# Kernel tuning notes

Measured on AMD Instinct MI355X. Metric: run time of the kernel, lower is better.

Reference implementation:

```python
import jax, jax.numpy as jnp
import numpy as np

N = 100000      # nodes
E = 1600000     # edges (avg degree 16)
EP = 500000     # pos/neg scored edges
DIN, DH, DOUT = 128, 128, 64


def setup_inputs() -> dict:
    key = jax.random.key(0)
    ks = jax.random.split(key, 8)
    x = jax.random.normal(ks[0], (N, DIN), jnp.float32)
    edge_index = jax.random.randint(ks[1], (2, E), 0, N)
    pos_edge_index = jax.random.randint(ks[2], (2, EP), 0, N)
    neg_edge_index = jax.random.randint(ks[3], (2, EP), 0, N)
    s = lambda k, sh: jax.random.normal(k, sh, jnp.float32) * 0.05
    return dict(
        x=x, edge_index=edge_index,
        pos_edge_index=pos_edge_index, neg_edge_index=neg_edge_index,
        W_l0=s(ks[4], (DIN, DH)), b_l0=jnp.zeros((DH,), jnp.float32), W_r0=s(ks[5], (DIN, DH)),
        W_l1=s(ks[6], (DH, DOUT)), b_l1=jnp.zeros((DOUT,), jnp.float32), W_r1=s(ks[7], (DH, DOUT)),
    )


def sage_conv(h, src, dst, W_l, b_l, W_r):
    # PyG SAGEConv (mean aggr): out_i = W_l @ mean_{j in N(i)} h_j + b_l + W_r @ h_i
    msg = h[src]                                                   # [E, d] gather
    agg = jax.ops.segment_sum(msg, dst, num_segments=h.shape[0])   # [N, d]
    deg = jax.ops.segment_sum(jnp.ones((src.shape[0],), h.dtype), dst, num_segments=h.shape[0])
    mean = agg / jnp.maximum(deg, 1.0)[:, None]
    return mean @ W_l + b_l + h @ W_r


def reference(x, edge_index, pos_edge_index, neg_edge_index,
              W_l0, b_l0, W_r0, W_l1, b_l1, W_r1):
    src, dst = edge_index[0], edge_index[1]
    h = sage_conv(x, src, dst, W_l0, b_l0, W_r0)
    h = jax.nn.relu(h)          # dropout is identity in eval mode
    h = sage_conv(h, src, dst, W_l1, b_l1, W_r1)
    pos_scores = (h[pos_edge_index[0]] * h[pos_edge_index[1]]).sum(axis=1)
    neg_scores = (h[neg_edge_index[0]] * h[neg_edge_index[1]]).sum(axis=1)
    return (pos_scores, neg_scores)
```

## Files before the change

kernel.cpp:

```cpp
#include <hip/hip_runtime.h>

#define NN 100000
#define EE 1600000
#define EPE 500000
#define NBINS 196
#define BCAP 12288
#define EPB 4096
#define NB1 391

typedef short bf8_t __attribute__((ext_vector_type(8)));
typedef float f4_t  __attribute__((ext_vector_type(4)));

__device__ __forceinline__ unsigned short f2bf(float f) {
    unsigned u = __float_as_uint(f);
    unsigned r = (u + 0x7fffu + ((u >> 16) & 1u)) >> 16;
    return (unsigned short)r;
}
__device__ __forceinline__ float bfl(unsigned u) { return __uint_as_float(u << 16); }
__device__ __forceinline__ float bfh(unsigned u) { return __uint_as_float(u & 0xffff0000u); }

__global__ __launch_bounds__(256) void binpass1_k(
    const int* __restrict__ src, const int* __restrict__ dst,
    int* __restrict__ bin_cnt, int* __restrict__ binbuf)
{
    __shared__ int cnt_l[NBINS];
    __shared__ int base_l[NBINS];
    int tid = threadIdx.x;
    int e0 = blockIdx.x * EPB;
    for (int i = tid; i < NBINS; i += 256) cnt_l[i] = 0;
    __syncthreads();

    int pk[16];
    #pragma unroll
    for (int i = 0; i < 16; ++i) {
        int e = e0 + tid + i * 256;
        pk[i] = -1;
        if (e < EE) {
            int b = dst[e] >> 9;
            int r = atomicAdd(&cnt_l[b], 1);
            pk[i] = (b << 16) | r;
        }
    }
    __syncthreads();
    for (int i = tid; i < NBINS; i += 256)
        base_l[i] = atomicAdd(&bin_cnt[i], cnt_l[i]);
    __syncthreads();

    #pragma unroll
    for (int i = 0; i < 16; ++i) {
        int e = e0 + tid + i * 256;
        if (e >= EE) continue;
        int b = pk[i] >> 16, r = pk[i] & 0xFFFF;
        int d = dst[e], s = src[e];
        binbuf[b * BCAP + base_l[b] + r] = ((d & 511) << 17) | s;
    }
}

__global__ void binscan_k(const int* __restrict__ bin_cnt, int* __restrict__ bin_base) {
    __shared__ int s[256];
    int tid = threadIdx.x;
    int v = (tid < NBINS) ? bin_cnt[tid] : 0;
    s[tid] = v;
    __syncthreads();
    #pragma unroll
    for (int off = 1; off < 256; off <<= 1) {
        int t = (tid >= off) ? s[tid - off] : 0;
        __syncthreads();
        s[tid] += t;
        __syncthreads();
    }
    if (tid < NBINS) bin_base[tid] = s[tid] - v;
}

__global__ __launch_bounds__(256) void binpass2_k(
    const int* __restrict__ binbuf, const int* __restrict__ bin_cnt,
    const int* __restrict__ bin_base, int* __restrict__ csr,
    int* __restrict__ row_ptr, float* __restrict__ invd)
{
    __shared__ int deg_l[512];
    __shared__ int off_l[512];
    __shared__ int cur_l[512];
    __shared__ int s[256];
    int tid = threadIdx.x;
    int b = blockIdx.x;
    int lo = b << 9;
    int n_here = min(512, NN - lo);
    int cnt = bin_cnt[b];
    int base = bin_base[b];
    const int* bb = binbuf + b * BCAP;

    deg_l[tid] = 0; deg_l[tid + 256] = 0;
    __syncthreads();
    for (int i = tid; i < cnt; i += 256)
        atomicAdd(&deg_l[bb[i] >> 17], 1);
    __syncthreads();

    int a0 = deg_l[2 * tid], a1 = deg_l[2 * tid + 1];
    s[tid] = a0 + a1;
    __syncthreads();
    #pragma unroll
    for (int off = 1; off < 256; off <<= 1) {
        int t = (tid >= off) ? s[tid - off] : 0;
        __syncthreads();
        s[tid] += t;
        __syncthreads();
    }
    int excl = s[tid] - (a0 + a1);
    off_l[2 * tid] = excl;
    off_l[2 * tid + 1] = excl + a0;
    cur_l[2 * tid] = excl;
    cur_l[2 * tid + 1] = excl + a0;
    __syncthreads();

    for (int j = tid; j < n_here; j += 256) {
        row_ptr[lo + j] = base + off_l[j];
        invd[lo + j] = 1.0f / fmaxf((float)deg_l[j], 1.0f);
    }
    if (tid == 0 && b == NBINS - 1) row_ptr[NN] = EE;

    for (int i = tid; i < cnt; i += 256) {
        int v = bb[i];
        int dstl = v >> 17, srcv = v & 0x1FFFF;
        int pos = atomicAdd(&cur_l[dstl], 1);
        csr[base + pos] = srcv;
    }
}

__global__ void pack_b_k(const float* __restrict__ Wl, const float* __restrict__ Wr,
                         int ncl, int ntot, unsigned short* __restrict__ Bp) {
    int t = blockIdx.x * 256 + threadIdx.x;
    if (t >= 4 * ntot * 4) return;
    int q = t & 3;
    int n = (t >> 2) % ntot;
    int kt = t / (4 * ntot);
    int ncr = ntot - ncl;
    unsigned short o[8];
    #pragma unroll
    for (int j = 0; j < 8; ++j) {
        int k = kt * 32 + q * 8 + j;
        float v = (n < ncl) ? Wl[(size_t)k * ncl + n] : Wr[(size_t)k * ncr + (n - ncl)];
        o[j] = f2bf(v);
    }
    uint4 w;
    w.x = (unsigned)o[0] | ((unsigned)o[1] << 16);
    w.y = (unsigned)o[2] | ((unsigned)o[3] << 16);
    w.z = (unsigned)o[4] | ((unsigned)o[5] << 16);
    w.w = (unsigned)o[6] | ((unsigned)o[7] << 16);
    *(uint4*)(Bp + (size_t)t * 8) = w;
}

template<int NCOLS, int TCOLS, bool AFP32>
__global__ __launch_bounds__(256) void gemm_k(
    const void* __restrict__ Av, const unsigned short* __restrict__ Bp,
    unsigned short* __restrict__ Tout, unsigned short* __restrict__ Rout)
{
    constexpr int NT = NCOLS / 16;
    int wave = threadIdx.x >> 6;
    int lane = threadIdx.x & 63;
    int ln = lane & 15, q = lane >> 4;
    int row0 = (blockIdx.x * 4 + wave) * 16;
    if (row0 >= NN) return;
    int arow = row0 + ln;

    f4_t acc[NT];
    #pragma unroll
    for (int nt = 0; nt < NT; ++nt) acc[nt] = (f4_t){0.f, 0.f, 0.f, 0.f};

    #pragma unroll
    for (int kt = 0; kt < 4; ++kt) {
        bf8_t a;
        if (AFP32) {
            const float* ap = (const float*)Av + (size_t)arow * 128 + kt * 32 + q * 8;
            f4_t a0 = *(const f4_t*)ap;
            f4_t a1 = *(const f4_t*)(ap + 4);
            #pragma unroll
            for (int j = 0; j < 4; ++j) {
                a[j]     = (short)f2bf(a0[j]);
                a[4 + j] = (short)f2bf(a1[j]);
            }
        } else {
            a = *(const bf8_t*)((const unsigned short*)Av + (size_t)arow * 128 + kt * 32 + q * 8);
        }
        const unsigned short* bb = Bp + (size_t)kt * NCOLS * 32 + (size_t)ln * 32 + q * 8;
        #pragma unroll
        for (int nt = 0; nt < NT; ++nt) {
            bf8_t b = *(const bf8_t*)(bb + nt * 512);
            acc[nt] = __builtin_amdgcn_mfma_f32_16x16x32_bf16(a, b, acc[nt], 0, 0, 0);
        }
    }

    #pragma unroll
    for (int nt = 0; nt < NT; ++nt) {
        #pragma unroll
        for (int r = 0; r < 4; ++r) {
            int row = row0 + q * 4 + r;
            int col = nt * 16 + ln;
            unsigned short v = f2bf(acc[nt][r]);
            if (col < TCOLS) Tout[(size_t)row * TCOLS + col] = v;
            else             Rout[(size_t)row * (NCOLS - TCOLS) + (col - TCOLS)] = v;
        }
    }
}

template<int LPNS, int WIDTH, bool RELU>
__global__ void gather_fuse_k(const unsigned short* __restrict__ feat,
                              const int* __restrict__ csr, const int* __restrict__ row_ptr,
                              const float* __restrict__ invd,
                              const unsigned short* __restrict__ rterm,
                              const float* __restrict__ bias,
                              unsigned short* __restrict__ hout)
{
    int t = blockIdx.x * 256 + threadIdx.x;
    int node = t >> LPNS;
    int lane = t & ((1 << LPNS) - 1);
    if (node >= NN) return;
    int e = row_ptr[node];
    int e1 = row_ptr[node + 1];

    float a0[8] = {0.f, 0.f, 0.f, 0.f, 0.f, 0.f, 0.f, 0.f};
    float a1[8] = {0.f, 0.f, 0.f, 0.f, 0.f, 0.f, 0.f, 0.f};
    for (; e + 1 < e1; e += 2) {
        int s0 = csr[e], s1 = csr[e + 1];
        uint4 v0 = *(const uint4*)(feat + (size_t)s0 * WIDTH + lane * 8);
        uint4 v1 = *(const uint4*)(feat + (size_t)s1 * WIDTH + lane * 8);
        a0[0] += bfl(v0.x); a0[1] += bfh(v0.x); a0[2] += bfl(v0.y); a0[3] += bfh(v0.y);
        a0[4] += bfl(v0.z); a0[5] += bfh(v0.z); a0[6] += bfl(v0.w); a0[7] += bfh(v0.w);
        a1[0] += bfl(v1.x); a1[1] += bfh(v1.x); a1[2] += bfl(v1.y); a1[3] += bfh(v1.y);
        a1[4] += bfl(v1.z); a1[5] += bfh(v1.z); a1[6] += bfl(v1.w); a1[7] += bfh(v1.w);
    }
    if (e < e1) {
        int s0 = csr[e];
        uint4 v0 = *(const uint4*)(feat + (size_t)s0 * WIDTH + lane * 8);
        a0[0] += bfl(v0.x); a0[1] += bfh(v0.x); a0[2] += bfl(v0.y); a0[3] += bfh(v0.y);
        a0[4] += bfl(v0.z); a0[5] += bfh(v0.z); a0[6] += bfl(v0.w); a0[7] += bfh(v0.w);
    }
    float inv = invd[node];
    uint4 rv = *(const uint4*)(rterm + (size_t)node * WIDTH + lane * 8);
    float rr[8] = {bfl(rv.x), bfh(rv.x), bfl(rv.y), bfh(rv.y),
                   bfl(rv.z), bfh(rv.z), bfl(rv.w), bfh(rv.w)};
    f4_t b0 = *(const f4_t*)(bias + lane * 8);
    f4_t b1 = *(const f4_t*)(bias + lane * 8 + 4);
    float o[8];
    #pragma unroll
    for (int j = 0; j < 8; ++j) {
        float bj = (j < 4) ? b0[j] : b1[j - 4];
        float v = (a0[j] + a1[j]) * inv + rr[j] + bj;
        o[j] = RELU ? fmaxf(v, 0.f) : v;
    }
    uint4 w;
    w.x = (unsigned)f2bf(o[0]) | ((unsigned)f2bf(o[1]) << 16);
    w.y = (unsigned)f2bf(o[2]) | ((unsigned)f2bf(o[3]) << 16);
    w.z = (unsigned)f2bf(o[4]) | ((unsigned)f2bf(o[5]) << 16);
    w.w = (unsigned)f2bf(o[6]) | ((unsigned)f2bf(o[7]) << 16);
    *(uint4*)(hout + (size_t)node * WIDTH + lane * 8) = w;
}

__global__ void score_k(const unsigned short* __restrict__ h2b, const int* __restrict__ pos,
                        const int* __restrict__ neg, float* __restrict__ out) {
    int t = blockIdx.x * 256 + threadIdx.x;
    int eg = t >> 3, l = t & 7;
    if (eg >= 2 * EPE) return;
    int a, b;
    if (eg < EPE) { a = pos[eg]; b = pos[EPE + eg]; }
    else { int e2 = eg - EPE; a = neg[e2]; b = neg[EPE + e2]; }
    uint4 va = *(const uint4*)(h2b + (size_t)a * 64 + l * 8);
    uint4 vb = *(const uint4*)(h2b + (size_t)b * 64 + l * 8);
    float p = bfl(va.x) * bfl(vb.x) + bfh(va.x) * bfh(vb.x)
            + bfl(va.y) * bfl(vb.y) + bfh(va.y) * bfh(vb.y)
            + bfl(va.z) * bfl(vb.z) + bfh(va.z) * bfh(vb.z)
            + bfl(va.w) * bfl(vb.w) + bfh(va.w) * bfh(vb.w);
    p += __shfl_xor(p, 1, 8);
    p += __shfl_xor(p, 2, 8);
    p += __shfl_xor(p, 4, 8);
    if (l == 0) out[eg] = p;
}

extern "C" void kernel_launch(void* const* d_in, const int* in_sizes, int n_in,
                              void* d_out, int out_size, void* d_ws, size_t ws_size,
                              hipStream_t stream) {
    const float* x   = (const float*)d_in[0];
    const int*   ei  = (const int*)d_in[1];
    const int*   pei = (const int*)d_in[2];
    const int*   nei = (const int*)d_in[3];
    const float* Wl0 = (const float*)d_in[4];
    const float* bl0 = (const float*)d_in[5];
    const float* Wr0 = (const float*)d_in[6];
    const float* Wl1 = (const float*)d_in[7];
    const float* bl1 = (const float*)d_in[8];
    const float* Wr1 = (const float*)d_in[9];
    float* out = (float*)d_out;

    char* ws = (char*)d_ws;
    size_t off = 0;
    auto alloc = [&](size_t bytes) {
        void* p = ws + off;
        off = (off + bytes + 255) & ~(size_t)255;
        return p;
    };
    float* invd     = (float*)alloc((size_t)NN * 4);
    int*   row_ptr  = (int*)  alloc((size_t)(NN + 1) * 4);
    int*   bin_cnt  = (int*)  alloc((size_t)NBINS * 4);
    int*   bin_base = (int*)  alloc((size_t)NBINS * 4);
    int*   binbuf   = (int*)  alloc((size_t)NBINS * BCAP * 4);
    int*   csr      = (int*)  alloc((size_t)EE * 4);
    unsigned short* Bp0 = (unsigned short*)alloc((size_t)4 * 256 * 4 * 8 * 2);
    unsigned short* Bp1 = (unsigned short*)alloc((size_t)4 * 128 * 4 * 8 * 2);
    unsigned short* t0  = (unsigned short*)alloc((size_t)NN * 128 * 2);
    unsigned short* r0b = (unsigned short*)alloc((size_t)NN * 128 * 2);
    unsigned short* h1b = (unsigned short*)alloc((size_t)NN * 128 * 2);
    unsigned short* t1  = t0;
    unsigned short* r1b = r0b;
    unsigned short* h2b = h1b;

    const int* src = ei;
    const int* dst = ei + EE;

    hipMemsetAsync(bin_cnt, 0, (size_t)NBINS * 4, stream);

    binpass1_k<<<NB1, 256, 0, stream>>>(src, dst, bin_cnt, binbuf);
    binscan_k<<<1, 256, 0, stream>>>(bin_cnt, bin_base);
    binpass2_k<<<NBINS, 256, 0, stream>>>(binbuf, bin_cnt, bin_base, csr, row_ptr, invd);

    pack_b_k<<<16, 256, 0, stream>>>(Wl0, Wr0, 128, 256, Bp0);
    pack_b_k<<<8, 256, 0, stream>>>(Wl1, Wr1, 64, 128, Bp1);

    gemm_k<256, 128, true><<<1563, 256, 0, stream>>>(x, Bp0, t0, r0b);
    gather_fuse_k<4, 128, true><<<(NN * 16) / 256, 256, 0, stream>>>(
        t0, csr, row_ptr, invd, r0b, bl0, h1b);

    gemm_k<128, 64, false><<<1563, 256, 0, stream>>>(h1b, Bp1, t1, r1b);
    gather_fuse_k<3, 64, false><<<(NN * 8) / 256, 256, 0, stream>>>(
        t1, csr, row_ptr, invd, r1b, bl1, h2b);

    score_k<<<(2 * EPE * 8) / 256, 256, 0, stream>>>(h2b, pei, nei, out);
}
```

Before: 345.3 us.

## Vectorize GEMM epilogue with permuted columns, fuse scan and packing, unroll gathers

Several unrelated changes land together. The GEMM epilogue now writes packed 16-byte rows in a permuted column order, and the weight and bias packing is permuted to match so the result stays correct. The bin scan kernel is folded into binpass2, which each block recomputes, and the two weight-pack launches are merged into one kernel that also permutes the biases. Binpass1 gets smaller blocks, the gather loop is unrolled to four neighbours, and score_k handles two edges per 8-lane group. The aim is fewer scattered 2-byte stores, fewer launches and more memory-level parallelism, at the cost of a redundant per-block scan and more intricate index bookkeeping.

```diff
diff --git a/kernel.cpp b/kernel.cpp
--- a/kernel.cpp
+++ b/kernel.cpp
@@ -5,8 +5,8 @@
 #define EPE 500000
 #define NBINS 196
 #define BCAP 12288
-#define EPB 4096
-#define NB1 391
+#define EPB 2048
+#define NB1 782
 
 typedef short bf8_t __attribute__((ext_vector_type(8)));
 typedef float f4_t  __attribute__((ext_vector_type(4)));
@@ -30,9 +30,9 @@
     for (int i = tid; i < NBINS; i += 256) cnt_l[i] = 0;
     __syncthreads();
 
-    int pk[16];
-    #pragma unroll
-    for (int i = 0; i < 16; ++i) {
+    int pk[8];
+    #pragma unroll
+    for (int i = 0; i < 8; ++i) {
         int e = e0 + tid + i * 256;
         pk[i] = -1;
         if (e < EE) {
@@ -47,7 +47,7 @@
     __syncthreads();
 
     #pragma unroll
-    for (int i = 0; i < 16; ++i) {
+    for (int i = 0; i < 8; ++i) {
         int e = e0 + tid + i * 256;
         if (e >= EE) continue;
         int b = pk[i] >> 16, r = pk[i] & 0xFFFF;
@@ -56,26 +56,9 @@
     }
 }
 
-__global__ void binscan_k(const int* __restrict__ bin_cnt, int* __restrict__ bin_base) {
-    __shared__ int s[256];
-    int tid = threadIdx.x;
-    int v = (tid < NBINS) ? bin_cnt[tid] : 0;
-    s[tid] = v;
-    __syncthreads();
-    #pragma unroll
-    for (int off = 1; off < 256; off <<= 1) {
-        int t = (tid >= off) ? s[tid - off] : 0;
-        __syncthreads();
-        s[tid] += t;
-        __syncthreads();
-    }
-    if (tid < NBINS) bin_base[tid] = s[tid] - v;
-}
-
 __global__ __launch_bounds__(256) void binpass2_k(
     const int* __restrict__ binbuf, const int* __restrict__ bin_cnt,
-    const int* __restrict__ bin_base, int* __restrict__ csr,
-    int* __restrict__ row_ptr, float* __restrict__ invd)
+    int* __restrict__ csr, int* __restrict__ row_ptr, float* __restrict__ invd)
 {
     __shared__ int deg_l[512];
     __shared__ int off_l[512];
@@ -85,18 +68,9 @@
     int b = blockIdx.x;
     int lo = b << 9;
     int n_here = min(512, NN - lo);
-    int cnt = bin_cnt[b];
-    int base = bin_base[b];
-    const int* bb = binbuf + b * BCAP;
-
-    deg_l[tid] = 0; deg_l[tid + 256] = 0;
-    __syncthreads();
-    for (int i = tid; i < cnt; i += 256)
-        atomicAdd(&deg_l[bb[i] >> 17], 1);
-    __syncthreads();
-
-    int a0 = deg_l[2 * tid], a1 = deg_l[2 * tid + 1];
-    s[tid] = a0 + a1;
+
+    int bc = (tid < NBINS) ? bin_cnt[tid] : 0;
+    s[tid] = bc;
     __syncthreads();
     #pragma unroll
     for (int off = 1; off < 256; off <<= 1) {
@@ -105,6 +79,27 @@
         s[tid] += t;
         __syncthreads();
     }
+    int base = (b == 0) ? 0 : s[b - 1];
+    int cnt = bin_cnt[b];
+    const int* bb = binbuf + b * BCAP;
+    __syncthreads();
+
+    deg_l[tid] = 0; deg_l[tid + 256] = 0;
+    __syncthreads();
+    for (int i = tid; i < cnt; i += 256)
+        atomicAdd(&deg_l[bb[i] >> 17], 1);
+    __syncthreads();
+
+    int a0 = deg_l[2 * tid], a1 = deg_l[2 * tid + 1];
+    s[tid] = a0 + a1;
+    __syncthreads();
+    #pragma unroll
+    for (int off = 1; off < 256; off <<= 1) {
+        int t = (tid >= off) ? s[tid - off] : 0;
+        __syncthreads();
+        s[tid] += t;
+        __syncthreads();
+    }
     int excl = s[tid] - (a0 + a1);
     off_l[2 * tid] = excl;
     off_l[2 * tid + 1] = excl + a0;
@@ -126,27 +121,56 @@
     }
 }
 
-__global__ void pack_b_k(const float* __restrict__ Wl, const float* __restrict__ Wr,
-                         int ncl, int ntot, unsigned short* __restrict__ Bp) {
+__global__ void pack_k(const float* __restrict__ Wl0, const float* __restrict__ Wr0,
+                       const float* __restrict__ Wl1, const float* __restrict__ Wr1,
+                       const float* __restrict__ bl0, const float* __restrict__ bl1,
+                       unsigned short* __restrict__ Bp0, unsigned short* __restrict__ Bp1,
+                       float* __restrict__ b0p, float* __restrict__ b1p)
+{
     int t = blockIdx.x * 256 + threadIdx.x;
-    if (t >= 4 * ntot * 4) return;
-    int q = t & 3;
-    int n = (t >> 2) % ntot;
-    int kt = t / (4 * ntot);
-    int ncr = ntot - ncl;
-    unsigned short o[8];
-    #pragma unroll
-    for (int j = 0; j < 8; ++j) {
-        int k = kt * 32 + q * 8 + j;
-        float v = (n < ncl) ? Wl[(size_t)k * ncl + n] : Wr[(size_t)k * ncr + (n - ncl)];
-        o[j] = f2bf(v);
-    }
-    uint4 w;
-    w.x = (unsigned)o[0] | ((unsigned)o[1] << 16);
-    w.y = (unsigned)o[2] | ((unsigned)o[3] << 16);
-    w.z = (unsigned)o[4] | ((unsigned)o[5] << 16);
-    w.w = (unsigned)o[6] | ((unsigned)o[7] << 16);
-    *(uint4*)(Bp + (size_t)t * 8) = w;
+    if (t < 4096) {
+        int q = t & 3;
+        int n = (t >> 2) & 255;
+        int kt = t >> 10;
+        unsigned short o[8];
+        #pragma unroll
+        for (int j = 0; j < 8; ++j) {
+            int k = kt * 32 + q * 8 + j;
+            float v = (n < 128) ? Wl0[(size_t)k * 128 + n] : Wr0[(size_t)k * 128 + (n - 128)];
+            o[j] = f2bf(v);
+        }
+        uint4 w;
+        w.x = (unsigned)o[0] | ((unsigned)o[1] << 16);
+        w.y = (unsigned)o[2] | ((unsigned)o[3] << 16);
+        w.z = (unsigned)o[4] | ((unsigned)o[5] << 16);
+        w.w = (unsigned)o[6] | ((unsigned)o[7] << 16);
+        *(uint4*)(Bp0 + (size_t)t * 8) = w;
+    } else if (t < 6144) {
+        int u = t - 4096;
+        int q = u & 3;
+        int n = (u >> 2) & 127;
+        int kt = u >> 9;
+        unsigned short o[8];
+        #pragma unroll
+        for (int j = 0; j < 8; ++j) {
+            int k = kt * 32 + q * 8 + j;
+            int c = ((k & 7) << 4) | (k >> 3);
+            float v = (n < 64) ? Wl1[(size_t)c * 64 + n] : Wr1[(size_t)c * 64 + (n - 64)];
+            o[j] = f2bf(v);
+        }
+        uint4 w;
+        w.x = (unsigned)o[0] | ((unsigned)o[1] << 16);
+        w.y = (unsigned)o[2] | ((unsigned)o[3] << 16);
+        w.z = (unsigned)o[4] | ((unsigned)o[5] << 16);
+        w.w = (unsigned)o[6] | ((unsigned)o[7] << 16);
+        *(uint4*)(Bp1 + (size_t)u * 8) = w;
+    } else if (t < 6144 + 128) {
+        int m = t - 6144;
+        b0p[m] = bl0[((m & 7) << 4) | (m >> 3)];
+    } else if (t < 6144 + 192) {
+        int m = t - 6272;
+        b1p[m] = bl1[((m & 3) << 4) | (m >> 2)];
+    }
 }
 
 template<int NCOLS, int TCOLS, bool AFP32>
@@ -155,6 +179,7 @@
     unsigned short* __restrict__ Tout, unsigned short* __restrict__ Rout)
 {
     constexpr int NT = NCOLS / 16;
+    constexpr int NTH = NCOLS / 32;
     int wave = threadIdx.x >> 6;
     int lane = threadIdx.x & 63;
     int ln = lane & 15, q = lane >> 4;
@@ -190,17 +215,39 @@
     }
 
     #pragma unroll
-    for (int nt = 0; nt < NT; ++nt) {
-        #pragma unroll
-        for (int r = 0; r < 4; ++r) {
-            int row = row0 + q * 4 + r;
-            int col = nt * 16 + ln;
-            unsigned short v = f2bf(acc[nt][r]);
-            if (col < TCOLS) Tout[(size_t)row * TCOLS + col] = v;
-            else             Rout[(size_t)row * (NCOLS - TCOLS) + (col - TCOLS)] = v;
-        }
-    }
-}
+    for (int r = 0; r < 4; ++r) {
+        int row = row0 + q * 4 + r;
+        if (NTH == 8) {
+            uint4 wt, wr;
+            wt.x = (unsigned)f2bf(acc[0][r]) | ((unsigned)f2bf(acc[1][r]) << 16);
+            wt.y = (unsigned)f2bf(acc[2][r]) | ((unsigned)f2bf(acc[3][r]) << 16);
+            wt.z = (unsigned)f2bf(acc[4][r]) | ((unsigned)f2bf(acc[5][r]) << 16);
+            wt.w = (unsigned)f2bf(acc[6][r]) | ((unsigned)f2bf(acc[7][r]) << 16);
+            wr.x = (unsigned)f2bf(acc[8][r])  | ((unsigned)f2bf(acc[9][r])  << 16);
+            wr.y = (unsigned)f2bf(acc[10][r]) | ((unsigned)f2bf(acc[11][r]) << 16);
+            wr.z = (unsigned)f2bf(acc[12][r]) | ((unsigned)f2bf(acc[13][r]) << 16);
+            wr.w = (unsigned)f2bf(acc[14][r]) | ((unsigned)f2bf(acc[15][r]) << 16);
+            *(uint4*)(Tout + (size_t)row * TCOLS + ln * 8) = wt;
+            *(uint4*)(Rout + (size_t)row * TCOLS + ln * 8) = wr;
+        } else {
+            uint2 wt, wr;
+            wt.x = (unsigned)f2bf(acc[0][r]) | ((unsigned)f2bf(acc[1][r]) << 16);
+            wt.y = (unsigned)f2bf(acc[2][r]) | ((unsigned)f2bf(acc[3][r]) << 16);
+            wr.x = (unsigned)f2bf(acc[4][r]) | ((unsigned)f2bf(acc[5][r]) << 16);
+            wr.y = (unsigned)f2bf(acc[6][r]) | ((unsigned)f2bf(acc[7][r]) << 16);
+            *(uint2*)(Tout + (size_t)row * TCOLS + ln * 4) = wt;
+            *(uint2*)(Rout + (size_t)row * TCOLS + ln * 4) = wr;
+        }
+    }
+}
+
+#define ACC8(a, v)                                                          \
+    do {                                                                    \
+        a[0] += bfl((v).x); a[1] += bfh((v).x);                             \
+        a[2] += bfl((v).y); a[3] += bfh((v).y);                             \
+        a[4] += bfl((v).z); a[5] += bfh((v).z);                             \
+        a[6] += bfl((v).w); a[7] += bfh((v).w);                             \
+    } while (0)
 
 template<int LPNS, int WIDTH, bool RELU>
 __global__ void gather_fuse_k(const unsigned short* __restrict__ feat,
@@ -216,23 +263,22 @@
     if (node >= NN) return;
     int e = row_ptr[node];
     int e1 = row_ptr[node + 1];
+    const unsigned short* fb = feat + (size_t)lane * 8;
 
     float a0[8] = {0.f, 0.f, 0.f, 0.f, 0.f, 0.f, 0.f, 0.f};
     float a1[8] = {0.f, 0.f, 0.f, 0.f, 0.f, 0.f, 0.f, 0.f};
-    for (; e + 1 < e1; e += 2) {
-        int s0 = csr[e], s1 = csr[e + 1];
-        uint4 v0 = *(const uint4*)(feat + (size_t)s0 * WIDTH + lane * 8);
-        uint4 v1 = *(const uint4*)(feat + (size_t)s1 * WIDTH + lane * 8);
-        a0[0] += bfl(v0.x); a0[1] += bfh(v0.x); a0[2] += bfl(v0.y); a0[3] += bfh(v0.y);
-        a0[4] += bfl(v0.z); a0[5] += bfh(v0.z); a0[6] += bfl(v0.w); a0[7] += bfh(v0.w);
-        a1[0] += bfl(v1.x); a1[1] += bfh(v1.x); a1[2] += bfl(v1.y); a1[3] += bfh(v1.y);
-        a1[4] += bfl(v1.z); a1[5] += bfh(v1.z); a1[6] += bfl(v1.w); a1[7] += bfh(v1.w);
-    }
-    if (e < e1) {
+    for (; e + 3 < e1; e += 4) {
+        int s0 = csr[e], s1 = csr[e + 1], s2 = csr[e + 2], s3 = csr[e + 3];
+        uint4 v0 = *(const uint4*)(fb + (size_t)s0 * WIDTH);
+        uint4 v1 = *(const uint4*)(fb + (size_t)s1 * WIDTH);
+        uint4 v2 = *(const uint4*)(fb + (size_t)s2 * WIDTH);
+        uint4 v3 = *(const uint4*)(fb + (size_t)s3 * WIDTH);
+        ACC8(a0, v0); ACC8(a1, v1); ACC8(a0, v2); ACC8(a1, v3);
+    }
+    for (; e < e1; ++e) {
         int s0 = csr[e];
-        uint4 v0 = *(const uint4*)(feat + (size_t)s0 * WIDTH + lane * 8);
-        a0[0] += bfl(v0.x); a0[1] += bfh(v0.x); a0[2] += bfl(v0.y); a0[3] += bfh(v0.y);
-        a0[4] += bfl(v0.z); a0[5] += bfh(v0.z); a0[6] += bfl(v0.w); a0[7] += bfh(v0.w);
+        uint4 v0 = *(const uint4*)(fb + (size_t)s0 * WIDTH);
+        ACC8(a0, v0);
     }
     float inv = invd[node];
     uint4 rv = *(const uint4*)(rterm + (size_t)node * WIDTH + lane * 8);
@@ -255,24 +301,39 @@
     *(uint4*)(hout + (size_t)node * WIDTH + lane * 8) = w;
 }
 
+__device__ __forceinline__ float dot8(uint4 va, uint4 vb) {
+    return bfl(va.x) * bfl(vb.x) + bfh(va.x) * bfh(vb.x)
+         + bfl(va.y) * bfl(vb.y) + bfh(va.y) * bfh(vb.y)
+         + bfl(va.z) * bfl(vb.z) + bfh(va.z) * bfh(vb.z)
+         + bfl(va.w) * bfl(vb.w) + bfh(va.w) * bfh(vb.w);
+}
+
 __global__ void score_k(const unsigned short* __restrict__ h2b, const int* __restrict__ pos,
                         const int* __restrict__ neg, float* __restrict__ out) {
     int t = blockIdx.x * 256 + threadIdx.x;
-    int eg = t >> 3, l = t & 7;
-    if (eg >= 2 * EPE) return;
-    int a, b;
-    if (eg < EPE) { a = pos[eg]; b = pos[EPE + eg]; }
-    else { int e2 = eg - EPE; a = neg[e2]; b = neg[EPE + e2]; }
-    uint4 va = *(const uint4*)(h2b + (size_t)a * 64 + l * 8);
-    uint4 vb = *(const uint4*)(h2b + (size_t)b * 64 + l * 8);
-    float p = bfl(va.x) * bfl(vb.x) + bfh(va.x) * bfh(vb.x)
-            + bfl(va.y) * bfl(vb.y) + bfh(va.y) * bfh(vb.y)
-            + bfl(va.z) * bfl(vb.z) + bfh(va.z) * bfh(vb.z)
-            + bfl(va.w) * bfl(vb.w) + bfh(va.w) * bfh(vb.w);
-    p += __shfl_xor(p, 1, 8);
-    p += __shfl_xor(p, 2, 8);
-    p += __shfl_xor(p, 4, 8);
-    if (l == 0) out[eg] = p;
+    int g = t >> 3, l = t & 7;
+    int eg0 = g * 2;
+    if (eg0 >= 2 * EPE) return;
+    int eg1 = eg0 + 1;
+    int a0i, b0i, a1i, b1i;
+    if (eg0 < EPE) { a0i = pos[eg0]; b0i = pos[EPE + eg0]; }
+    else { int e2 = eg0 - EPE; a0i = neg[e2]; b0i = neg[EPE + e2]; }
+    if (eg1 < EPE) { a1i = pos[eg1]; b1i = pos[EPE + eg1]; }
+    else { int e2 = eg1 - EPE; a1i = neg[e2]; b1i = neg[EPE + e2]; }
+    const unsigned short* hb = h2b + (size_t)l * 8;
+    uint4 va0 = *(const uint4*)(hb + (size_t)a0i * 64);
+    uint4 vb0 = *(const uint4*)(hb + (size_t)b0i * 64);
+    uint4 va1 = *(const uint4*)(hb + (size_t)a1i * 64);
+    uint4 vb1 = *(const uint4*)(hb + (size_t)b1i * 64);
+    float p0 = dot8(va0, vb0);
+    float p1 = dot8(va1, vb1);
+    p0 += __shfl_xor(p0, 1, 8);
+    p1 += __shfl_xor(p1, 1, 8);
+    p0 += __shfl_xor(p0, 2, 8);
+    p1 += __shfl_xor(p1, 2, 8);
+    p0 += __shfl_xor(p0, 4, 8);
+    p1 += __shfl_xor(p1, 4, 8);
+    if (l == 0) { out[eg0] = p0; out[eg1] = p1; }
 }
 
 extern "C" void kernel_launch(void* const* d_in, const int* in_sizes, int n_in,
@@ -300,11 +361,12 @@
     float* invd     = (float*)alloc((size_t)NN * 4);
     int*   row_ptr  = (int*)  alloc((size_t)(NN + 1) * 4);
     int*   bin_cnt  = (int*)  alloc((size_t)NBINS * 4);
-    int*   bin_base = (int*)  alloc((size_t)NBINS * 4);
     int*   binbuf   = (int*)  alloc((size_t)NBINS * BCAP * 4);
     int*   csr      = (int*)  alloc((size_t)EE * 4);
-    unsigned short* Bp0 = (unsigned short*)alloc((size_t)4 * 256 * 4 * 8 * 2);
-    unsigned short* Bp1 = (unsigned short*)alloc((size_t)4 * 128 * 4 * 8 * 2);
+    unsigned short* Bp0 = (unsigned short*)alloc((size_t)4096 * 8 * 2);
+    unsigned short* Bp1 = (unsigned short*)alloc((size_t)2048 * 8 * 2);
+    float* b0p = (float*)alloc(128 * 4);
+    float* b1p = (float*)alloc(64 * 4);
     unsigned short* t0  = (unsigned short*)alloc((size_t)NN * 128 * 2);
     unsigned short* r0b = (unsigned short*)alloc((size_t)NN * 128 * 2);
     unsigned short* h1b = (unsigned short*)alloc((size_t)NN * 128 * 2);
@@ -318,19 +380,17 @@
     hipMemsetAsync(bin_cnt, 0, (size_t)NBINS * 4, stream);
 
     binpass1_k<<<NB1, 256, 0, stream>>>(src, dst, bin_cnt, binbuf);
-    binscan_k<<<1, 256, 0, stream>>>(bin_cnt, bin_base);
-    binpass2_k<<<NBINS, 256, 0, stream>>>(binbuf, bin_cnt, bin_base, csr, row_ptr, invd);
-
-    pack_b_k<<<16, 256, 0, stream>>>(Wl0, Wr0, 128, 256, Bp0);
-    pack_b_k<<<8, 256, 0, stream>>>(Wl1, Wr1, 64, 128, Bp1);
+    binpass2_k<<<NBINS, 256, 0, stream>>>(binbuf, bin_cnt, csr, row_ptr, invd);
+
+    pack_k<<<25, 256, 0, stream>>>(Wl0, Wr0, Wl1, Wr1, bl0, bl1, Bp0, Bp1, b0p, b1p);
 
     gemm_k<256, 128, true><<<1563, 256, 0, stream>>>(x, Bp0, t0, r0b);
-    gather_fuse_k<4, 128, true><<<(NN * 16) / 256, 256, 0, stream>>>(
-        t0, csr, row_ptr, invd, r0b, bl0, h1b);
+    gather_fuse_k<4, 128, true><<<(NN * 16 + 255) / 256, 256, 0, stream>>>(
+        t0, csr, row_ptr, invd, r0b, b0p, h1b);
 
     gemm_k<128, 64, false><<<1563, 256, 0, stream>>>(h1b, Bp1, t1, r1b);
-    gather_fuse_k<3, 64, false><<<(NN * 8) / 256, 256, 0, stream>>>(
-        t1, csr, row_ptr, invd, r1b, bl1, h2b);
-
-    score_k<<<(2 * EPE * 8) / 256, 256, 0, stream>>>(h2b, pei, nei, out);
-}
+    gather_fuse_k<3, 64, false><<<(NN * 8 + 255) / 256, 256, 0, stream>>>(
+        t1, csr, row_ptr, invd, r1b, b1p, h2b);
+
+    score_k<<<(EPE * 8 + 255) / 256, 256, 0, stream>>>(h2b, pei, nei, out);
+}
```

Result: faster. 334.6 us (-3.1%).
